# Performance work log

Hardware: AMD Instinct MI355X
Metric: run time of the kernel (lower is better)

The kernel has to match this reference:

```python
import jax, jax.numpy as jnp
import numpy as np
import math

D_MODEL = 1024
NUM_HEADS = 16
HEAD_DIM = D_MODEL // NUM_HEADS


def setup_inputs() -> dict:
    key = jax.random.key(0)
    ks = jax.random.split(key, 9)
    B, T = 4, 2048
    s = 1.0 / math.sqrt(D_MODEL)
    return {
        "x": jax.random.normal(ks[0], (B, T, D_MODEL), dtype=jnp.float32),
        "Wq": jax.random.normal(ks[1], (D_MODEL, D_MODEL), dtype=jnp.float32) * s,
        "bq": jnp.zeros((D_MODEL,), dtype=jnp.float32),
        "Wk": jax.random.normal(ks[2], (D_MODEL, D_MODEL), dtype=jnp.float32) * s,
        "bk": jnp.zeros((D_MODEL,), dtype=jnp.float32),
        "Wv": jax.random.normal(ks[3], (D_MODEL, D_MODEL), dtype=jnp.float32) * s,
        "bv": jnp.zeros((D_MODEL,), dtype=jnp.float32),
        "Wo": jax.random.normal(ks[4], (D_MODEL, D_MODEL), dtype=jnp.float32) * s,
        "bo": jnp.zeros((D_MODEL,), dtype=jnp.float32),
    }


def reference(x, Wq, bq, Wk, bk, Wv, bv, Wo, bo):
    # x: [B, T, D]. Weights stored as [in, out] (torch Linear weight transposed).
    B, T, D = x.shape
    H, Hd = NUM_HEADS, HEAD_DIM

    def heads(w, b):
        # [B,T,D] -> [B,H,T,Hd]
        return (x @ w + b).reshape(B, T, H, Hd).transpose(0, 2, 1, 3)

    q = heads(Wq, bq)
    k = heads(Wk, bk)
    v = heads(Wv, bv)

    scores = jnp.einsum("bhqd,bhkd->bhqk", q, k) / math.sqrt(Hd)
    attn = jax.nn.softmax(scores, axis=-1)  # dropout is identity in eval mode
    ctx = jnp.einsum("bhqk,bhkd->bhqd", attn, v)
    ctx = ctx.transpose(0, 2, 1, 3).reshape(B, T, D)
    return ctx @ Wo + bo
```

## Files before the change

kernel.cpp:

```cpp
#include <hip/hip_runtime.h>
#include <hip/hip_bf16.h>

#define D_MODEL 1024
#define NHEADS  16
#define HD      64
#define BATCH   4
#define SEQ     2048
#define MROWS   (BATCH*SEQ)

typedef __attribute__((ext_vector_type(8))) short bf16x8;
typedef __attribute__((ext_vector_type(4))) float f32x4;
typedef __attribute__((ext_vector_type(16))) float f32x16;
typedef __attribute__((ext_vector_type(4))) unsigned int u32x4;
typedef __attribute__((ext_vector_type(2))) unsigned int u32x2;
#define MFMA16(a,b,c) __builtin_amdgcn_mfma_f32_16x16x32_bf16(a,b,c,0,0,0)
#define MFMA32(a,b,c) __builtin_amdgcn_mfma_f32_32x32x16_bf16(a,b,c,0,0,0)

__device__ __forceinline__ short f2bf(float f) {
    __hip_bfloat16 h = __float2bfloat16(f);
    return *reinterpret_cast<short*>(&h);
}
__device__ __forceinline__ unsigned cvtpk(float a, float b) {
    unsigned r; asm("v_cvt_pk_bf16_f32 %0, %1, %2" : "=v"(r) : "v"(a), "v"(b)); return r;
}
__device__ __forceinline__ float fexp2(float x) {
    float r; asm("v_exp_f32 %0, %1" : "=v"(r) : "v"(x)); return r;
}

typedef const __attribute__((address_space(1))) unsigned char* gas_t;
typedef __attribute__((address_space(3))) unsigned char* las_t;
#define GLD16(gp, lp) __builtin_amdgcn_global_load_lds((gas_t)(gp), (las_t)(lp), 16, 0, 0)

__global__ __launch_bounds__(256) void round_x(const float* __restrict__ in, short* __restrict__ out) {
    const size_t i = ((size_t)blockIdx.x * 256 + threadIdx.x) * 8;
    float4 a = *reinterpret_cast<const float4*>(&in[i]);
    float4 b = *reinterpret_cast<const float4*>(&in[i + 4]);
    bf16x8 v;
    v[0]=f2bf(a.x); v[1]=f2bf(a.y); v[2]=f2bf(a.z); v[3]=f2bf(a.w);
    v[4]=f2bf(b.x); v[5]=f2bf(b.y); v[6]=f2bf(b.z); v[7]=f2bf(b.w);
    *reinterpret_cast<bf16x8*>(&out[i]) = v;
}

__global__ __launch_bounds__(256) void transpose_w(
    const float* __restrict__ W, short* __restrict__ out)
{
    __shared__ float tile[64][65];
    const int bk = blockIdx.y * 64;
    const int bn = blockIdx.x * 64;
    const int t = threadIdx.x;
    const int r = t >> 2, c0 = (t & 3) * 16;
    #pragma unroll
    for (int i = 0; i < 16; i += 4) {
        float4 v = *reinterpret_cast<const float4*>(&W[(size_t)(bk + r) * D_MODEL + bn + c0 + i]);
        tile[r][c0+i] = v.x; tile[r][c0+i+1] = v.y; tile[r][c0+i+2] = v.z; tile[r][c0+i+3] = v.w;
    }
    __syncthreads();
    bf16x8 H0, H1;
    #pragma unroll
    for (int i = 0; i < 8; i++) { H0[i] = f2bf(tile[c0 + i][r]); H1[i] = f2bf(tile[c0 + 8 + i][r]); }
    short* hp = &out[(size_t)(bn + r) * D_MODEL + bk + c0];
    *reinterpret_cast<bf16x8*>(hp) = H0;
    *reinterpret_cast<bf16x8*>(hp + 8) = H1;
}

__global__ __launch_bounds__(256) void gemm_qkv(
    const short* __restrict__ A,
    const short* __restrict__ WqT, const short* __restrict__ WkT, const short* __restrict__ WvT,
    const float* __restrict__ bq, const float* __restrict__ bk, const float* __restrict__ bv,
    short* __restrict__ qo, short* __restrict__ ko, short* __restrict__ vo,
    const float qscale)
{
    __shared__ short As[2][128 * 32];
    __shared__ short Bs[2][128 * 32];
    const int tid = threadIdx.x, wave = tid >> 6, lane = tid & 63;
    const int g = lane >> 4, li = lane & 15;
    const int lin = blockIdx.x + blockIdx.y * 24;
    const int swz = (lin & 7) * 192 + (lin >> 3);
    const int bx = swz % 24, by = swz / 24;
    const int which = bx >> 3;
    const int bm = by * 128, bn = (bx & 7) * 128;
    const int wr = wave >> 1, wc = wave & 1;
    const int lrow = lane >> 2, lcol = (lane & 3) * 8;

    const short* BT = (which == 0) ? WqT : (which == 1) ? WkT : WvT;
    const float* bias = (which == 0) ? bq : (which == 1) ? bk : bv;
    short* out = (which == 0) ? qo : (which == 1) ? ko : vo;
    const float scale = (which == 0) ? qscale : 1.0f;

    f32x4 acc[4][4];
    #pragma unroll
    for (int i = 0; i < 4; i++)
        #pragma unroll
        for (int j = 0; j < 4; j++)
            #pragma unroll
            for (int r = 0; r < 4; r++) acc[i][j][r] = 0.f;

    #pragma unroll
    for (int c = 0; c < 2; c++) {
        const int ch = wave + c * 4;
        const int row = ch * 16 + lrow;
        GLD16(&A [(size_t)(bm + row) * D_MODEL + lcol], &As[0][ch * 512]);
        GLD16(&BT[(size_t)(bn + row) * D_MODEL + lcol], &Bs[0][ch * 512]);
    }

    const int NSTEP = D_MODEL / 32;
    for (int ks = 0; ks < NSTEP; ks++) {
        const int cur = ks & 1;
        if (ks + 1 < NSTEP) {
            const int k0 = (ks + 1) * 32;
            #pragma unroll
            for (int c = 0; c < 2; c++) {
                const int ch = wave + c * 4;
                const int row = ch * 16 + lrow;
                GLD16(&A [(size_t)(bm + row) * D_MODEL + k0 + lcol], &As[cur ^ 1][ch * 512]);
                GLD16(&BT[(size_t)(bn + row) * D_MODEL + k0 + lcol], &Bs[cur ^ 1][ch * 512]);
            }
            asm volatile("s_waitcnt vmcnt(4)" ::: "memory");
        } else {
            asm volatile("s_waitcnt vmcnt(0)" ::: "memory");
        }
        __builtin_amdgcn_s_barrier();
        __builtin_amdgcn_sched_barrier(0);

        bf16x8 af[4], bfr[4];
        #pragma unroll
        for (int mi = 0; mi < 4; mi++) af[mi]  = *reinterpret_cast<const bf16x8*>(&As[cur][(wr * 64 + mi * 16 + li) * 32 + g * 8]);
        #pragma unroll
        for (int ni = 0; ni < 4; ni++) bfr[ni] = *reinterpret_cast<const bf16x8*>(&Bs[cur][(wc * 64 + ni * 16 + li) * 32 + g * 8]);
        #pragma unroll
        for (int mi = 0; mi < 4; mi++)
            #pragma unroll
            for (int ni = 0; ni < 4; ni++)
                acc[mi][ni] = MFMA16(af[mi], bfr[ni], acc[mi][ni]);
        __builtin_amdgcn_s_barrier();
    }

    #pragma unroll
    for (int mi = 0; mi < 4; mi++) {
        #pragma unroll
        for (int r = 0; r < 4; r++) {
            const int m = bm + wr * 64 + mi * 16 + g * 4 + r;
            const int b = m >> 11, t = m & (SEQ - 1);
            #pragma unroll
            for (int ni = 0; ni < 4; ni++) {
                const int n = bn + wc * 64 + ni * 16 + li;
                const float val = (acc[mi][ni][r] + bias[n]) * scale;
                const int h = n >> 6, hd = n & 63;
                if (which != 2) out[((size_t)((b * NHEADS + h) * SEQ + t)) * HD + hd] = f2bf(val);
                else            out[((size_t)((b * NHEADS + h) * HD + hd)) * SEQ + t] = f2bf(val);
            }
        }
    }
}

__global__ __launch_bounds__(256) void gemm_wo(
    const short* __restrict__ A, const short* __restrict__ BT,
    const float* __restrict__ bias, float* __restrict__ out)
{
    __shared__ short As[2][128 * 32];
    __shared__ short Bs[2][128 * 32];
    const int tid = threadIdx.x, wave = tid >> 6, lane = tid & 63;
    const int g = lane >> 4, li = lane & 15;
    const int lin = blockIdx.x + blockIdx.y * 8;
    const int swz = (lin & 7) * 64 + (lin >> 3);
    const int bm = (swz >> 3) * 128, bn = (swz & 7) * 128;
    const int wr = wave >> 1, wc = wave & 1;
    const int lrow = lane >> 2, lcol = (lane & 3) * 8;

    f32x4 acc[4][4];
    #pragma unroll
    for (int i = 0; i < 4; i++)
        #pragma unroll
        for (int j = 0; j < 4; j++)
            #pragma unroll
            for (int r = 0; r < 4; r++) acc[i][j][r] = 0.f;

    #pragma unroll
    for (int c = 0; c < 2; c++) {
        const int ch = wave + c * 4;
        const int row = ch * 16 + lrow;
        GLD16(&A [(size_t)(bm + row) * D_MODEL + lcol], &As[0][ch * 512]);
        GLD16(&BT[(size_t)(bn + row) * D_MODEL + lcol], &Bs[0][ch * 512]);
    }

    const int NSTEP = D_MODEL / 32;
    for (int ks = 0; ks < NSTEP; ks++) {
        const int cur = ks & 1;
        if (ks + 1 < NSTEP) {
            const int k0 = (ks + 1) * 32;
            #pragma unroll
            for (int c = 0; c < 2; c++) {
                const int ch = wave + c * 4;
                const int row = ch * 16 + lrow;
                GLD16(&A [(size_t)(bm + row) * D_MODEL + k0 + lcol], &As[cur ^ 1][ch * 512]);
                GLD16(&BT[(size_t)(bn + row) * D_MODEL + k0 + lcol], &Bs[cur ^ 1][ch * 512]);
            }
            asm volatile("s_waitcnt vmcnt(4)" ::: "memory");
        } else {
            asm volatile("s_waitcnt vmcnt(0)" ::: "memory");
        }
        __builtin_amdgcn_s_barrier();
        __builtin_amdgcn_sched_barrier(0);

        bf16x8 af[4], bfr[4];
        #pragma unroll
        for (int mi = 0; mi < 4; mi++) af[mi]  = *reinterpret_cast<const bf16x8*>(&As[cur][(wr * 64 + mi * 16 + li) * 32 + g * 8]);
        #pragma unroll
        for (int ni = 0; ni < 4; ni++) bfr[ni] = *reinterpret_cast<const bf16x8*>(&Bs[cur][(wc * 64 + ni * 16 + li) * 32 + g * 8]);
        #pragma unroll
        for (int mi = 0; mi < 4; mi++)
            #pragma unroll
            for (int ni = 0; ni < 4; ni++)
                acc[mi][ni] = MFMA16(af[mi], bfr[ni], acc[mi][ni]);
        __builtin_amdgcn_s_barrier();
    }

    #pragma unroll
    for (int mi = 0; mi < 4; mi++) {
        #pragma unroll
        for (int r = 0; r < 4; r++) {
            const int m = bm + wr * 64 + mi * 16 + g * 4 + r;
            #pragma unroll
            for (int ni = 0; ni < 4; ni++) {
                const int n = bn + wc * 64 + ni * 16 + li;
                out[(size_t)m * D_MODEL + n] = acc[mi][ni][r] + bias[n];
            }
        }
    }
}

__global__ __launch_bounds__(256) void attn_mfma(
    const short* __restrict__ q, const short* __restrict__ k,
    const short* __restrict__ vT, short* __restrict__ ch)
{
    __shared__ short Ks[2][64 * 64];
    __shared__ short Vs[2][64 * 64];

    const int bh = blockIdx.x;
    const int b  = bh >> 4, h = bh & (NHEADS - 1);
    const int qt = blockIdx.y;
    const int tid = threadIdx.x;
    const int wave = tid >> 6, lane = tid & 63;
    const int ql = lane & 31;
    const int hi = lane >> 5;
    const int qand7 = ql & 7;

    const short* qp = q + ((size_t)bh * SEQ + qt * 128 + wave * 32 + ql) * HD;
    const bf16x8 qf0 = *reinterpret_cast<const bf16x8*>(qp + 0  + hi * 8);
    const bf16x8 qf1 = *reinterpret_cast<const bf16x8*>(qp + 16 + hi * 8);
    const bf16x8 qf2 = *reinterpret_cast<const bf16x8*>(qp + 32 + hi * 8);
    const bf16x8 qf3 = *reinterpret_cast<const bf16x8*>(qp + 48 + hi * 8);

    f32x16 o0, o1;
    #pragma unroll
    for (int i = 0; i < 16; i++) { o0[i] = 0.f; o1[i] = 0.f; }
    float lR = 0.f;

    const short* kbase = k  + (size_t)bh * SEQ * HD;
    const short* vbase = vT + (size_t)bh * HD * SEQ;

    const int srow = lane >> 3;
    const int gsl  = (lane & 7) ^ srow;
    const int q0 = wave * 2, q1 = wave * 2 + 1;

    GLD16(kbase + (q0 * 8 + srow) * HD + gsl * 8, &Ks[0][q0 * 512]);
    GLD16(kbase + (q1 * 8 + srow) * HD + gsl * 8, &Ks[0][q1 * 512]);
    GLD16(vbase + (size_t)(q0 * 8 + srow) * SEQ + gsl * 8, &Vs[0][q0 * 512]);
    GLD16(vbase + (size_t)(q1 * 8 + srow) * SEQ + gsl * 8, &Vs[0][q1 * 512]);

    const int NT = SEQ / 64;
    for (int kt = 0; kt < NT; kt++) {
        const int cur = kt & 1;
        if (kt + 1 < NT) {
            const short* kg = kbase + (size_t)(kt + 1) * 64 * HD;
            const short* vg = vbase + (kt + 1) * 64;
            GLD16(kg + (q0 * 8 + srow) * HD + gsl * 8, &Ks[cur ^ 1][q0 * 512]);
            GLD16(kg + (q1 * 8 + srow) * HD + gsl * 8, &Ks[cur ^ 1][q1 * 512]);
            GLD16(vg + (size_t)(q0 * 8 + srow) * SEQ + gsl * 8, &Vs[cur ^ 1][q0 * 512]);
            GLD16(vg + (size_t)(q1 * 8 + srow) * SEQ + gsl * 8, &Vs[cur ^ 1][q1 * 512]);
            asm volatile("s_waitcnt vmcnt(4)" ::: "memory");
        } else {
            asm volatile("s_waitcnt vmcnt(0)" ::: "memory");
        }
        __builtin_amdgcn_s_barrier();
        __builtin_amdgcn_sched_barrier(0);

        const short* Kb = Ks[cur];
        const short* Vb = Vs[cur];

        f32x16 s0, s1;
        #pragma unroll
        for (int i = 0; i < 16; i++) { s0[i] = 0.f; s1[i] = 0.f; }
        __builtin_amdgcn_s_setprio(1);
#define QK_STEP(DC, QF) do { \
            const int ksl = (((DC) * 2 + hi) ^ qand7) * 8; \
            const bf16x8 ka0 = *reinterpret_cast<const bf16x8*>(&Kb[ql * 64 + ksl]); \
            const bf16x8 ka1 = *reinterpret_cast<const bf16x8*>(&Kb[(32 + ql) * 64 + ksl]); \
            s0 = MFMA32(ka0, QF, s0); \
            s1 = MFMA32(ka1, QF, s1); \
        } while (0)
        QK_STEP(0, qf0); QK_STEP(1, qf1); QK_STEP(2, qf2); QK_STEP(3, qf3);
#undef QK_STEP
        __builtin_amdgcn_s_setprio(0);

        float sum = 0.f;
        #pragma unroll
        for (int i = 0; i < 16; i++) { s0[i] = fexp2(s0[i]); sum += s0[i]; }
        #pragma unroll
        for (int i = 0; i < 16; i++) { s1[i] = fexp2(s1[i]); sum += s1[i]; }
        sum += __shfl_xor(sum, 32);
        lR += sum;

        __builtin_amdgcn_s_setprio(1);
#define PV_STEP(KB, SS, B) do { \
            const unsigned a0 = cvtpk(SS[(B) + 0], SS[(B) + 1]); \
            const unsigned a1 = cvtpk(SS[(B) + 2], SS[(B) + 3]); \
            const unsigned a2 = cvtpk(SS[(B) + 4], SS[(B) + 5]); \
            const unsigned a3 = cvtpk(SS[(B) + 6], SS[(B) + 7]); \
            const u32x2 r02 = __builtin_amdgcn_permlane32_swap(a0, a2, false, false); \
            const u32x2 r13 = __builtin_amdgcn_permlane32_swap(a1, a3, false, false); \
            u32x4 wv; \
            wv[0] = r02[0]; wv[1] = r13[0]; wv[2] = r02[1]; wv[3] = r13[1]; \
            const bf16x8 pf = __builtin_bit_cast(bf16x8, wv); \
            const int vsl = (((KB) * 2 + hi) ^ qand7) * 8; \
            const bf16x8 vf0 = *reinterpret_cast<const bf16x8*>(&Vb[ql * 64 + vsl]); \
            const bf16x8 vf1 = *reinterpret_cast<const bf16x8*>(&Vb[(32 + ql) * 64 + vsl]); \
            o0 = MFMA32(vf0, pf, o0); \
            o1 = MFMA32(vf1, pf, o1); \
        } while (0)
        PV_STEP(0, s0, 0); PV_STEP(1, s0, 8); PV_STEP(2, s1, 0); PV_STEP(3, s1, 8);
#undef PV_STEP
        __builtin_amdgcn_s_setprio(0);

        __builtin_amdgcn_s_barrier();
    }

    const float inv = 1.0f / lR;
    const int t = qt * 128 + wave * 32 + ql;
    const size_t base = ((size_t)(b * SEQ + t)) * D_MODEL + h * HD;
    #pragma unroll
    for (int blk = 0; blk < 4; blk++) {
        uint2 w0, w1;
        w0.x = cvtpk(o0[4*blk + 0] * inv, o0[4*blk + 1] * inv);
        w0.y = cvtpk(o0[4*blk + 2] * inv, o0[4*blk + 3] * inv);
        w1.x = cvtpk(o1[4*blk + 0] * inv, o1[4*blk + 1] * inv);
        w1.y = cvtpk(o1[4*blk + 2] * inv, o1[4*blk + 3] * inv);
        *reinterpret_cast<uint2*>(&ch[base + 8*blk + 4*hi])      = w0;
        *reinterpret_cast<uint2*>(&ch[base + 32 + 8*blk + 4*hi]) = w1;
    }
}

extern "C" void kernel_launch(void* const* d_in, const int* in_sizes, int n_in,
                              void* d_out, int out_size, void* d_ws, size_t ws_size,
                              hipStream_t stream) {
    const float* x  = (const float*)d_in[0];
    const float* Wq = (const float*)d_in[1];
    const float* bq = (const float*)d_in[2];
    const float* Wk = (const float*)d_in[3];
    const float* bk = (const float*)d_in[4];
    const float* Wv = (const float*)d_in[5];
    const float* bv = (const float*)d_in[6];
    const float* Wo = (const float*)d_in[7];
    const float* bo = (const float*)d_in[8];

    const size_t S1 = (size_t)MROWS * D_MODEL;
    const size_t SW = (size_t)D_MODEL * D_MODEL;
    short* xb  = (short*)d_ws;
    short* qb  = xb + S1;
    short* kb  = qb + S1;
    short* vb  = kb + S1;
    short* chb = vb + S1;
    short* WqT = chb + S1;
    short* WkT = WqT + SW;
    short* WvT = WkT + SW;
    short* WoT = WvT + SW;

    round_x<<<4096, 256, 0, stream>>>(x, xb);
    dim3 tg(16, 16);
    transpose_w<<<tg, 256, 0, stream>>>(Wq, WqT);
    transpose_w<<<tg, 256, 0, stream>>>(Wk, WkT);
    transpose_w<<<tg, 256, 0, stream>>>(Wv, WvT);
    transpose_w<<<tg, 256, 0, stream>>>(Wo, WoT);

    const float QSCALE = 0.125f * 1.4426950408889634f;
    gemm_qkv<<<dim3(24, 64), 256, 0, stream>>>(xb, WqT, WkT, WvT, bq, bk, bv,
                                               qb, kb, vb, QSCALE);
    attn_mfma<<<dim3(BATCH * NHEADS, SEQ / 128), 256, 0, stream>>>(qb, kb, vb, chb);
    gemm_wo<<<dim3(8, 64), 256, 0, stream>>>(chb, WoT, bo, (float*)d_out);
}
```

Measured before the change: 239.6 us.

## Triple-buffer GEMM and attention loads, fuse prep kernels, packed softmax sums

Merges the x rounding and four weight-transpose launches into one prep kernel, cutting the launch count. Moves both GEMMs and the attention kernel from double to triple buffering in LDS, issuing loads two steps ahead with adjusted waitcnt thresholds to hide more memory latency. In attention, the first QK MFMA now accumulates into a shared zero vector instead of re-zeroing the score registers, and the row sum uses packed f32 adds. Larger LDS footprint may lower occupancy.

```diff
diff --git a/kernel.cpp b/kernel.cpp
--- a/kernel.cpp
+++ b/kernel.cpp
@@ -11,6 +11,7 @@
 typedef __attribute__((ext_vector_type(8))) short bf16x8;
 typedef __attribute__((ext_vector_type(4))) float f32x4;
 typedef __attribute__((ext_vector_type(16))) float f32x16;
+typedef __attribute__((ext_vector_type(2))) float f32x2;
 typedef __attribute__((ext_vector_type(4))) unsigned int u32x4;
 typedef __attribute__((ext_vector_type(2))) unsigned int u32x2;
 #define MFMA16(a,b,c) __builtin_amdgcn_mfma_f32_16x16x32_bf16(a,b,c,0,0,0)
@@ -26,28 +27,42 @@
 __device__ __forceinline__ float fexp2(float x) {
     float r; asm("v_exp_f32 %0, %1" : "=v"(r) : "v"(x)); return r;
 }
+__device__ __forceinline__ f32x2 pkadd(f32x2 a, f32x2 b) {
+    f32x2 d; asm("v_pk_add_f32 %0, %1, %2" : "=v"(d) : "v"(a), "v"(b)); return d;
+}
+#define SH2(V,I) __builtin_shufflevector(V, V, I, (I)+1)
 
 typedef const __attribute__((address_space(1))) unsigned char* gas_t;
 typedef __attribute__((address_space(3))) unsigned char* las_t;
 #define GLD16(gp, lp) __builtin_amdgcn_global_load_lds((gas_t)(gp), (las_t)(lp), 16, 0, 0)
 
-__global__ __launch_bounds__(256) void round_x(const float* __restrict__ in, short* __restrict__ out) {
-    const size_t i = ((size_t)blockIdx.x * 256 + threadIdx.x) * 8;
-    float4 a = *reinterpret_cast<const float4*>(&in[i]);
-    float4 b = *reinterpret_cast<const float4*>(&in[i + 4]);
-    bf16x8 v;
-    v[0]=f2bf(a.x); v[1]=f2bf(a.y); v[2]=f2bf(a.z); v[3]=f2bf(a.w);
-    v[4]=f2bf(b.x); v[5]=f2bf(b.y); v[6]=f2bf(b.z); v[7]=f2bf(b.w);
-    *reinterpret_cast<bf16x8*>(&out[i]) = v;
-}
-
-__global__ __launch_bounds__(256) void transpose_w(
-    const float* __restrict__ W, short* __restrict__ out)
+__global__ __launch_bounds__(256) void prep(
+    const float* __restrict__ x,
+    const float* __restrict__ Wq, const float* __restrict__ Wk,
+    const float* __restrict__ Wv, const float* __restrict__ Wo,
+    short* __restrict__ xb,
+    short* __restrict__ WqT, short* __restrict__ WkT,
+    short* __restrict__ WvT, short* __restrict__ WoT)
 {
     __shared__ float tile[64][65];
-    const int bk = blockIdx.y * 64;
-    const int bn = blockIdx.x * 64;
+    const int bid = blockIdx.x;
     const int t = threadIdx.x;
+    if (bid < 4096) {
+        const size_t i = ((size_t)bid * 256 + t) * 8;
+        float4 a = *reinterpret_cast<const float4*>(&x[i]);
+        float4 b = *reinterpret_cast<const float4*>(&x[i + 4]);
+        bf16x8 v;
+        v[0]=f2bf(a.x); v[1]=f2bf(a.y); v[2]=f2bf(a.z); v[3]=f2bf(a.w);
+        v[4]=f2bf(b.x); v[5]=f2bf(b.y); v[6]=f2bf(b.z); v[7]=f2bf(b.w);
+        *reinterpret_cast<bf16x8*>(&xb[i]) = v;
+        return;
+    }
+    const int tt = bid - 4096;
+    const int w = tt >> 8;
+    const int tl = tt & 255;
+    const int bn = (tl & 15) * 64, bk = (tl >> 4) * 64;
+    const float* W = (w==0)?Wq:(w==1)?Wk:(w==2)?Wv:Wo;
+    short* out     = (w==0)?WqT:(w==1)?WkT:(w==2)?WvT:WoT;
     const int r = t >> 2, c0 = (t & 3) * 16;
     #pragma unroll
     for (int i = 0; i < 16; i += 4) {
@@ -70,8 +85,8 @@
     short* __restrict__ qo, short* __restrict__ ko, short* __restrict__ vo,
     const float qscale)
 {
-    __shared__ short As[2][128 * 32];
-    __shared__ short Bs[2][128 * 32];
+    __shared__ short As[3][128 * 32];
+    __shared__ short Bs[3][128 * 32];
     const int tid = threadIdx.x, wave = tid >> 6, lane = tid & 63;
     const int g = lane >> 4, li = lane & 15;
     const int lin = blockIdx.x + blockIdx.y * 24;
@@ -95,26 +110,27 @@
             #pragma unroll
             for (int r = 0; r < 4; r++) acc[i][j][r] = 0.f;
 
-    #pragma unroll
-    for (int c = 0; c < 2; c++) {
-        const int ch = wave + c * 4;
-        const int row = ch * 16 + lrow;
-        GLD16(&A [(size_t)(bm + row) * D_MODEL + lcol], &As[0][ch * 512]);
-        GLD16(&BT[(size_t)(bn + row) * D_MODEL + lcol], &Bs[0][ch * 512]);
-    }
+#define STAGEG(KS, BUF) do { \
+        const int k0_ = (KS) * 32; \
+        _Pragma("unroll") \
+        for (int c = 0; c < 2; c++) { \
+            const int ch = wave + c * 4; \
+            const int row = ch * 16 + lrow; \
+            GLD16(&A [(size_t)(bm + row) * D_MODEL + k0_ + lcol], &As[BUF][ch * 512]); \
+            GLD16(&BT[(size_t)(bn + row) * D_MODEL + k0_ + lcol], &Bs[BUF][ch * 512]); \
+        } \
+    } while (0)
+
+    STAGEG(0, 0);
+    STAGEG(1, 1);
 
     const int NSTEP = D_MODEL / 32;
     for (int ks = 0; ks < NSTEP; ks++) {
-        const int cur = ks & 1;
-        if (ks + 1 < NSTEP) {
-            const int k0 = (ks + 1) * 32;
-            #pragma unroll
-            for (int c = 0; c < 2; c++) {
-                const int ch = wave + c * 4;
-                const int row = ch * 16 + lrow;
-                GLD16(&A [(size_t)(bm + row) * D_MODEL + k0 + lcol], &As[cur ^ 1][ch * 512]);
-                GLD16(&BT[(size_t)(bn + row) * D_MODEL + k0 + lcol], &Bs[cur ^ 1][ch * 512]);
-            }
+        const int cur = ks % 3;
+        if (ks + 2 < NSTEP) {
+            STAGEG(ks + 2, (ks + 2) % 3);
+            asm volatile("s_waitcnt vmcnt(8)" ::: "memory");
+        } else if (ks + 1 < NSTEP) {
             asm volatile("s_waitcnt vmcnt(4)" ::: "memory");
         } else {
             asm volatile("s_waitcnt vmcnt(0)" ::: "memory");
@@ -134,6 +150,7 @@
                 acc[mi][ni] = MFMA16(af[mi], bfr[ni], acc[mi][ni]);
         __builtin_amdgcn_s_barrier();
     }
+#undef STAGEG
 
     #pragma unroll
     for (int mi = 0; mi < 4; mi++) {
@@ -157,8 +174,8 @@
     const short* __restrict__ A, const short* __restrict__ BT,
     const float* __restrict__ bias, float* __restrict__ out)
 {
-    __shared__ short As[2][128 * 32];
-    __shared__ short Bs[2][128 * 32];
+    __shared__ short As[3][128 * 32];
+    __shared__ short Bs[3][128 * 32];
     const int tid = threadIdx.x, wave = tid >> 6, lane = tid & 63;
     const int g = lane >> 4, li = lane & 15;
     const int lin = blockIdx.x + blockIdx.y * 8;
@@ -175,26 +192,27 @@
             #pragma unroll
             for (int r = 0; r < 4; r++) acc[i][j][r] = 0.f;
 
-    #pragma unroll
-    for (int c = 0; c < 2; c++) {
-        const int ch = wave + c * 4;
-        const int row = ch * 16 + lrow;
-        GLD16(&A [(size_t)(bm + row) * D_MODEL + lcol], &As[0][ch * 512]);
-        GLD16(&BT[(size_t)(bn + row) * D_MODEL + lcol], &Bs[0][ch * 512]);
-    }
+#define STAGEG(KS, BUF) do { \
+        const int k0_ = (KS) * 32; \
+        _Pragma("unroll") \
+        for (int c = 0; c < 2; c++) { \
+            const int ch = wave + c * 4; \
+            const int row = ch * 16 + lrow; \
+            GLD16(&A [(size_t)(bm + row) * D_MODEL + k0_ + lcol], &As[BUF][ch * 512]); \
+            GLD16(&BT[(size_t)(bn + row) * D_MODEL + k0_ + lcol], &Bs[BUF][ch * 512]); \
+        } \
+    } while (0)
+
+    STAGEG(0, 0);
+    STAGEG(1, 1);
 
     const int NSTEP = D_MODEL / 32;
     for (int ks = 0; ks < NSTEP; ks++) {
-        const int cur = ks & 1;
-        if (ks + 1 < NSTEP) {
-            const int k0 = (ks + 1) * 32;
-            #pragma unroll
-            for (int c = 0; c < 2; c++) {
-                const int ch = wave + c * 4;
-                const int row = ch * 16 + lrow;
-                GLD16(&A [(size_t)(bm + row) * D_MODEL + k0 + lcol], &As[cur ^ 1][ch * 512]);
-                GLD16(&BT[(size_t)(bn + row) * D_MODEL + k0 + lcol], &Bs[cur ^ 1][ch * 512]);
-            }
+        const int cur = ks % 3;
+        if (ks + 2 < NSTEP) {
+            STAGEG(ks + 2, (ks + 2) % 3);
+            asm volatile("s_waitcnt vmcnt(8)" ::: "memory");
+        } else if (ks + 1 < NSTEP) {
             asm volatile("s_waitcnt vmcnt(4)" ::: "memory");
         } else {
             asm volatile("s_waitcnt vmcnt(0)" ::: "memory");
@@ -214,6 +232,7 @@
                 acc[mi][ni] = MFMA16(af[mi], bfr[ni], acc[mi][ni]);
         __builtin_amdgcn_s_barrier();
     }
+#undef STAGEG
 
     #pragma unroll
     for (int mi = 0; mi < 4; mi++) {
@@ -233,8 +252,8 @@
     const short* __restrict__ q, const short* __restrict__ k,
     const short* __restrict__ vT, short* __restrict__ ch)
 {
-    __shared__ short Ks[2][64 * 64];
-    __shared__ short Vs[2][64 * 64];
+    __shared__ short Ks[3][64 * 64];
+    __shared__ short Vs[3][64 * 64];
 
     const int bh = blockIdx.x;
     const int b  = bh >> 4, h = bh & (NHEADS - 1);
@@ -251,9 +270,9 @@
     const bf16x8 qf2 = *reinterpret_cast<const bf16x8*>(qp + 32 + hi * 8);
     const bf16x8 qf3 = *reinterpret_cast<const bf16x8*>(qp + 48 + hi * 8);
 
-    f32x16 o0, o1;
-    #pragma unroll
-    for (int i = 0; i < 16; i++) { o0[i] = 0.f; o1[i] = 0.f; }
+    f32x16 o0, o1, Z;
+    #pragma unroll
+    for (int i = 0; i < 16; i++) { o0[i] = 0.f; o1[i] = 0.f; Z[i] = 0.f; }
     float lR = 0.f;
 
     const short* kbase = k  + (size_t)bh * SEQ * HD;
@@ -263,21 +282,25 @@
     const int gsl  = (lane & 7) ^ srow;
     const int q0 = wave * 2, q1 = wave * 2 + 1;
 
-    GLD16(kbase + (q0 * 8 + srow) * HD + gsl * 8, &Ks[0][q0 * 512]);
-    GLD16(kbase + (q1 * 8 + srow) * HD + gsl * 8, &Ks[0][q1 * 512]);
-    GLD16(vbase + (size_t)(q0 * 8 + srow) * SEQ + gsl * 8, &Vs[0][q0 * 512]);
-    GLD16(vbase + (size_t)(q1 * 8 + srow) * SEQ + gsl * 8, &Vs[0][q1 * 512]);
+#define STAGE(T, BUF) do { \
+        const short* kg_ = kbase + (size_t)(T) * 64 * HD; \
+        const short* vg_ = vbase + (size_t)(T) * 64; \
+        GLD16(kg_ + (q0 * 8 + srow) * HD + gsl * 8, &Ks[BUF][q0 * 512]); \
+        GLD16(kg_ + (q1 * 8 + srow) * HD + gsl * 8, &Ks[BUF][q1 * 512]); \
+        GLD16(vg_ + (size_t)(q0 * 8 + srow) * SEQ + gsl * 8, &Vs[BUF][q0 * 512]); \
+        GLD16(vg_ + (size_t)(q1 * 8 + srow) * SEQ + gsl * 8, &Vs[BUF][q1 * 512]); \
+    } while (0)
+
+    STAGE(0, 0);
+    STAGE(1, 1);
 
     const int NT = SEQ / 64;
     for (int kt = 0; kt < NT; kt++) {
-        const int cur = kt & 1;
-        if (kt + 1 < NT) {
-            const short* kg = kbase + (size_t)(kt + 1) * 64 * HD;
-            const short* vg = vbase + (kt + 1) * 64;
-            GLD16(kg + (q0 * 8 + srow) * HD + gsl * 8, &Ks[cur ^ 1][q0 * 512]);
-            GLD16(kg + (q1 * 8 + srow) * HD + gsl * 8, &Ks[cur ^ 1][q1 * 512]);
-            GLD16(vg + (size_t)(q0 * 8 + srow) * SEQ + gsl * 8, &Vs[cur ^ 1][q0 * 512]);
-            GLD16(vg + (size_t)(q1 * 8 + srow) * SEQ + gsl * 8, &Vs[cur ^ 1][q1 * 512]);
+        const int cur = kt % 3;
+        if (kt + 2 < NT) {
+            STAGE(kt + 2, (kt + 2) % 3);
+            asm volatile("s_waitcnt vmcnt(8)" ::: "memory");
+        } else if (kt + 1 < NT) {
             asm volatile("s_waitcnt vmcnt(4)" ::: "memory");
         } else {
             asm volatile("s_waitcnt vmcnt(0)" ::: "memory");
@@ -289,27 +312,42 @@
         const short* Vb = Vs[cur];
 
         f32x16 s0, s1;
-        #pragma unroll
-        for (int i = 0; i < 16; i++) { s0[i] = 0.f; s1[i] = 0.f; }
         __builtin_amdgcn_s_setprio(1);
-#define QK_STEP(DC, QF) do { \
+#define QK_STEP(DC, QF, C0, C1) do { \
             const int ksl = (((DC) * 2 + hi) ^ qand7) * 8; \
             const bf16x8 ka0 = *reinterpret_cast<const bf16x8*>(&Kb[ql * 64 + ksl]); \
             const bf16x8 ka1 = *reinterpret_cast<const bf16x8*>(&Kb[(32 + ql) * 64 + ksl]); \
-            s0 = MFMA32(ka0, QF, s0); \
-            s1 = MFMA32(ka1, QF, s1); \
+            s0 = MFMA32(ka0, QF, C0); \
+            s1 = MFMA32(ka1, QF, C1); \
         } while (0)
-        QK_STEP(0, qf0); QK_STEP(1, qf1); QK_STEP(2, qf2); QK_STEP(3, qf3);
+        QK_STEP(0, qf0, Z, Z);
+        QK_STEP(1, qf1, s0, s1);
+        QK_STEP(2, qf2, s0, s1);
+        QK_STEP(3, qf3, s0, s1);
 #undef QK_STEP
         __builtin_amdgcn_s_setprio(0);
 
-        float sum = 0.f;
-        #pragma unroll
-        for (int i = 0; i < 16; i++) { s0[i] = fexp2(s0[i]); sum += s0[i]; }
-        #pragma unroll
-        for (int i = 0; i < 16; i++) { s1[i] = fexp2(s1[i]); sum += s1[i]; }
-        sum += __shfl_xor(sum, 32);
-        lR += sum;
+        #pragma unroll
+        for (int i = 0; i < 16; i++) s0[i] = fexp2(s0[i]);
+        #pragma unroll
+        for (int i = 0; i < 16; i++) s1[i] = fexp2(s1[i]);
+        {
+            f32x2 p0 = pkadd(SH2(s0, 0), SH2(s0, 2));
+            f32x2 p1 = pkadd(SH2(s0, 4), SH2(s0, 6));
+            f32x2 p2 = pkadd(SH2(s0, 8), SH2(s0, 10));
+            f32x2 p3 = pkadd(SH2(s0, 12), SH2(s0, 14));
+            f32x2 p4 = pkadd(SH2(s1, 0), SH2(s1, 2));
+            f32x2 p5 = pkadd(SH2(s1, 4), SH2(s1, 6));
+            f32x2 p6 = pkadd(SH2(s1, 8), SH2(s1, 10));
+            f32x2 p7 = pkadd(SH2(s1, 12), SH2(s1, 14));
+            p0 = pkadd(p0, p1); p2 = pkadd(p2, p3);
+            p4 = pkadd(p4, p5); p6 = pkadd(p6, p7);
+            p0 = pkadd(p0, p2); p4 = pkadd(p4, p6);
+            p0 = pkadd(p0, p4);
+            float sum = p0[0] + p0[1];
+            sum += __shfl_xor(sum, 32);
+            lR += sum;
+        }
 
         __builtin_amdgcn_s_setprio(1);
 #define PV_STEP(KB, SS, B) do { \
@@ -334,6 +372,7 @@
 
         __builtin_amdgcn_s_barrier();
     }
+#undef STAGE
 
     const float inv = 1.0f / lR;
     const int t = qt * 128 + wave * 32 + ql;
@@ -375,12 +414,7 @@
     short* WvT = WkT + SW;
     short* WoT = WvT + SW;
 
-    round_x<<<4096, 256, 0, stream>>>(x, xb);
-    dim3 tg(16, 16);
-    transpose_w<<<tg, 256, 0, stream>>>(Wq, WqT);
-    transpose_w<<<tg, 256, 0, stream>>>(Wk, WkT);
-    transpose_w<<<tg, 256, 0, stream>>>(Wv, WvT);
-    transpose_w<<<tg, 256, 0, stream>>>(Wo, WoT);
+    prep<<<5120, 256, 0, stream>>>(x, Wq, Wk, Wv, Wo, xb, WqT, WkT, WvT, WoT);
 
     const float QSCALE = 0.125f * 1.4426950408889634f;
     gemm_qkv<<<dim3(24, 64), 256, 0, stream>>>(xb, WqT, WkT, WvT, bq, bk, bv,
```

Measured after the change: 220.7 us. -7.9%, faster.
